# Kernel optimization log

Measured on AMD Instinct MI355X. Metric: run time of the kernel, lower is better.

Reference implementation:

```python
import jax, jax.numpy as jnp
import numpy as np

N = 100000      # nodes
E = 1600000     # edges (avg degree 16)
IN_DIM = 256
HID = 128
EPS = 0.3


def setup_inputs() -> dict:
    key = jax.random.key(0)
    ks = jax.random.split(key, 6)
    x = jax.random.normal(ks[0], (N, IN_DIM), dtype=jnp.float32)
    # edges without self-loops (dst = src + nonzero offset mod N)
    src = jax.random.randint(ks[1], (E,), 0, N)
    off = jax.random.randint(ks[2], (E,), 1, N)
    dst = (src + off) % N
    edge_index = jnp.stack([src, dst]).astype(jnp.int32)
    # xavier_normal_ with gain=1.414 for t1 and gate
    g1 = 1.414 * np.sqrt(2.0 / (IN_DIM + HID))
    w1 = (jax.random.normal(ks[3], (HID, IN_DIM)) * g1).astype(jnp.float32)
    b1 = jnp.zeros((HID,), jnp.float32)
    gg = 1.414 * np.sqrt(2.0 / (2 * HID + 1))
    gate_w = (jax.random.normal(ks[4], (1, 2 * HID)) * gg).astype(jnp.float32)
    gate_b = jnp.zeros((1,), jnp.float32)
    return dict(x=x, edge_index=edge_index, w1=w1, b1=b1, gate_w=gate_w, gate_b=gate_b)


def reference(x, edge_index, w1, b1, gate_w, gate_b):
    src, dst = edge_index[0], edge_index[1]
    # in-degree based symmetric norm, deg clamped to >= 1
    deg = jax.ops.segment_sum(jnp.ones((E,), jnp.float32), dst, num_segments=N)
    norm = jnp.clip(deg, 1.0) ** -0.5  # [N]

    h = jax.nn.relu(x @ w1.T + b1)     # [N, HID] (dropout p=0 / eval -> identity)
    raw = h

    # gate([h_dst, h_src]) decomposed: concat @ W^T = h_dst @ w_d + h_src @ w_s
    w_d, w_s = gate_w[0, :HID], gate_w[0, HID:]
    a_dst = h @ w_d                    # [N]
    a_src = h @ w_s                    # [N]
    g = jnp.tanh(a_dst[dst] + a_src[src] + gate_b[0])   # [E] per-edge gate
    e = g * norm[dst] * norm[src]                        # [E]

    # u_mul_e + sum: gather src features, weight, scatter-add to dst
    z = jax.ops.segment_sum(h[src] * e[:, None], dst, num_segments=N)  # [N, HID]
    return EPS * raw + z
```

## Files before the change

### kernel.cpp

```cpp
#include <hip/hip_runtime.h>
#include <math.h>
#include <stdint.h>

#define N_NODES 100000
#define N_EDGES 1600000
#define IN_DIM  256
#define HID     128
#define EPS_C   0.3f

#define NPB      128
#define NBKT     782
#define NBKT_P   784
#define BCAP     3072
#define S1_CHUNK 4096
#define S1_BLOCKS 391
#define GC(b)    ((b) * 16)

#define PK_SRC(p)  ((p) & 0x1FFFF)
#define PK_LI(p)   ((p) >> 17)

typedef __attribute__((ext_vector_type(8))) __bf16 bf16x8;
typedef __attribute__((ext_vector_type(4))) float  f32x4;
typedef __attribute__((ext_vector_type(8))) unsigned short ushort8;

static __device__ __forceinline__ unsigned short f2bf(float f) {
    unsigned u = __float_as_uint(f);
    unsigned r = (u + 0x7fffu + ((u >> 16) & 1u)) >> 16;
    return (unsigned short)r;
}
static __device__ __forceinline__ float bf2f(unsigned short s) {
    return __uint_as_float((unsigned)s << 16);
}
static __device__ __forceinline__ float fast_tanh(float x) {
    float e = __builtin_exp2f(x * 2.8853900817779268f);
    return 1.0f - 2.0f / (e + 1.0f);
}

__global__ __launch_bounds__(256) void convert_w1_kernel(const float* __restrict__ w1,
                                                         unsigned short* __restrict__ w1b) {
    int i = blockIdx.x * 256 + threadIdx.x;
    if (i * 4 >= HID * IN_DIM) return;
    float4 v = *(const float4*)&w1[i * 4];
    ushort4 r;
    r.x = f2bf(v.x); r.y = f2bf(v.y); r.z = f2bf(v.z); r.w = f2bf(v.w);
    *(ushort4*)&w1b[i * 4] = r;
}

__global__ __launch_bounds__(512) void partition_kernel(const int* __restrict__ src,
                                                        const int* __restrict__ dst,
                                                        int* __restrict__ gcur,
                                                        int* __restrict__ ebuf) {
    __shared__ int hist[NBKT_P];
    __shared__ int cur[NBKT_P];

    int t = threadIdx.x;
    for (int i = t; i < NBKT_P; i += 512) hist[i] = 0;
    __syncthreads();

    int base4 = blockIdx.x * (S1_CHUNK / 4);
    int rem4  = N_EDGES / 4 - base4;

    int4 sv[2], dv[2];
#pragma unroll
    for (int j = 0; j < 2; j++) {
        int i4 = j * 512 + t;
        if (i4 < rem4) {
            sv[j] = *(const int4*)&src[(base4 + i4) * 4];
            dv[j] = *(const int4*)&dst[(base4 + i4) * 4];
        } else {
            dv[j] = make_int4(-1, -1, -1, -1);
        }
    }
#pragma unroll
    for (int j = 0; j < 2; j++) {
        if (dv[j].x >= 0) {
            atomicAdd(&hist[dv[j].x >> 7], 1);
            atomicAdd(&hist[dv[j].y >> 7], 1);
            atomicAdd(&hist[dv[j].z >> 7], 1);
            atomicAdd(&hist[dv[j].w >> 7], 1);
        }
    }
    __syncthreads();

    if (t < NBKT_P / 2) {
        int h0 = hist[2 * t], h1 = hist[2 * t + 1];
        if (h0 > 0) cur[2 * t]     = atomicAdd(&gcur[GC(2 * t)], h0);
        if (h1 > 0) cur[2 * t + 1] = atomicAdd(&gcur[GC(2 * t + 1)], h1);
    }
    __syncthreads();

#pragma unroll
    for (int j = 0; j < 2; j++) {
        if (dv[j].x >= 0) {
            int b, p;
            b = dv[j].x >> 7; p = atomicAdd(&cur[b], 1);
            if (p < BCAP) ebuf[(size_t)b * BCAP + p] = ((dv[j].x & (NPB - 1)) << 17) | sv[j].x;
            b = dv[j].y >> 7; p = atomicAdd(&cur[b], 1);
            if (p < BCAP) ebuf[(size_t)b * BCAP + p] = ((dv[j].y & (NPB - 1)) << 17) | sv[j].y;
            b = dv[j].z >> 7; p = atomicAdd(&cur[b], 1);
            if (p < BCAP) ebuf[(size_t)b * BCAP + p] = ((dv[j].z & (NPB - 1)) << 17) | sv[j].z;
            b = dv[j].w >> 7; p = atomicAdd(&cur[b], 1);
            if (p < BCAP) ebuf[(size_t)b * BCAP + p] = ((dv[j].w & (NPB - 1)) << 17) | sv[j].w;
        }
    }
}

__global__ __launch_bounds__(512) void deg_kernel(const int* __restrict__ gcur,
                                                  const int* __restrict__ ebuf,
                                                  int2* __restrict__ rs2,
                                                  float* __restrict__ nrm) {
    __shared__ int dcnt[NPB];
    __shared__ int s[NPB];
    int b = blockIdx.x;
    int t = threadIdx.x;
    if (t < NPB) dcnt[t] = 0;
    __syncthreads();

    int ecnt = gcur[GC(b)];
    if (ecnt > BCAP) ecnt = BCAP;
    for (int j = t; j < ecnt; j += 512)
        atomicAdd(&dcnt[PK_LI(ebuf[(size_t)b * BCAP + j])], 1);
    __syncthreads();

    int v = 0;
    if (t < NPB) { v = dcnt[t]; s[t] = v; }
    __syncthreads();
    for (int off = 1; off < NPB; off <<= 1) {
        int a = (t < NPB && t >= off) ? s[t - off] : 0;
        __syncthreads();
        if (t < NPB) s[t] += a;
        __syncthreads();
    }

    int nbase = b * NPB;
    int nn = N_NODES - nbase;
    if (nn > NPB) nn = NPB;
    if (t < nn) {
        int incl = s[t];
        rs2[nbase + t] = make_int2(b * BCAP + incl - v, b * BCAP + incl);
        nrm[nbase + t] = rsqrtf(fmaxf((float)v, 1.0f));
    }
}

__global__ __launch_bounds__(512, 4) void gemm_kernel(const float* __restrict__ x,
                                                      const unsigned short* __restrict__ w1b,
                                                      const float* __restrict__ b1,
                                                      const float* __restrict__ gw,
                                                      const float* __restrict__ nrm,
                                                      unsigned short* __restrict__ h,
                                                      float2* __restrict__ pd_pack,
                                                      float2* __restrict__ ps_pack) {
    __shared__ unsigned short Bs[HID * IN_DIM];

    int tid  = threadIdx.x;
    int bm   = blockIdx.x * 128;
    int wv   = tid >> 6;
    int lane = tid & 63;
    int col  = lane & 15;
    int kq   = lane >> 4;

    {
        int n  = tid >> 2;
        int c0 = tid & 3;
        const unsigned short* srcp = &w1b[n * IN_DIM];
#pragma unroll
        for (int j = 0; j < 8; j++) {
            int c = c0 + 4 * j;
            *(ushort8*)((char*)Bs + n * 512 + ((c ^ (n & 7)) * 16)) =
                *(const ushort8*)&srcp[c * 8];
        }
    }

    f32x4 acc[8];
#pragma unroll
    for (int nf = 0; nf < 8; nf++) acc[nf] = (f32x4){0.f, 0.f, 0.f, 0.f};

    int row  = bm + wv * 16 + col;
    bool rok = row < N_NODES;
    const float* ap = &x[(size_t)row * IN_DIM + kq * 8];

    bf16x8 af[8];
#pragma unroll
    for (int i = 0; i < 8; i++) {
        float4 a0 = {0, 0, 0, 0}, a1 = {0, 0, 0, 0};
        if (rok) {
            a0 = *(const float4*)(ap + 32 * i);
            a1 = *(const float4*)(ap + 32 * i + 4);
        }
        ushort8 av;
        av[0] = f2bf(a0.x); av[1] = f2bf(a0.y); av[2] = f2bf(a0.z); av[3] = f2bf(a0.w);
        av[4] = f2bf(a1.x); av[5] = f2bf(a1.y); av[6] = f2bf(a1.z); av[7] = f2bf(a1.w);
        af[i] = *(bf16x8*)&av;
    }

    __syncthreads();

#pragma unroll
    for (int i = 0; i < 8; i++) {
        int swz = (4 * i + kq) ^ (col & 7);
#pragma unroll
        for (int nf = 0; nf < 8; nf++) {
            int n = nf * 16 + col;
            bf16x8 bfrag = *(bf16x8*)((char*)Bs + n * 512 + swz * 16);
            acc[nf] = __builtin_amdgcn_mfma_f32_16x16x32_bf16(af[i], bfrag, acc[nf], 0, 0, 0);
        }
    }

    float bias[8], wd[8], wsv[8];
#pragma unroll
    for (int nf = 0; nf < 8; nf++) {
        bias[nf] = b1[nf * 16 + col];
        wd[nf]   = gw[nf * 16 + col];
        wsv[nf]  = gw[HID + nf * 16 + col];
    }
#pragma unroll
    for (int r = 0; r < 4; r++) {
        int gm = bm + wv * 16 + kq * 4 + r;
        float pd = 0.f, ps = 0.f;
        bool ok = (gm < N_NODES);
#pragma unroll
        for (int nf = 0; nf < 8; nf++) {
            float v = fmaxf(acc[nf][r] + bias[nf], 0.f);
            pd = fmaf(v, wd[nf], pd);
            ps = fmaf(v, wsv[nf], ps);
            if (ok) h[(size_t)gm * HID + nf * 16 + col] = f2bf(v);
        }
#pragma unroll
        for (int m = 1; m < 16; m <<= 1) {
            pd += __shfl_xor(pd, m);
            ps += __shfl_xor(ps, m);
        }
        if (ok && col == 0) {
            float nv = nrm[gm];
            pd_pack[gm] = make_float2(pd, nv);
            ps_pack[gm] = make_float2(ps, nv);
        }
    }
}

__global__ __launch_bounds__(512) void scatter2_kernel(const int* __restrict__ gcur,
                                                       const int* __restrict__ ebuf,
                                                       const int2* __restrict__ rs2,
                                                       const float2* __restrict__ pd_pack,
                                                       const float2* __restrict__ ps_pack,
                                                       const float* __restrict__ gb,
                                                       int2* __restrict__ epack) {
    __shared__ int    curs[NPB];
    __shared__ float2 pdl[NPB];
    int b = blockIdx.x;
    int t = threadIdx.x;
    int nbase = b * NPB;
    int nn = N_NODES - nbase;
    if (nn > NPB) nn = NPB;
    if (t < nn) {
        curs[t] = rs2[nbase + t].x;
        pdl[t]  = pd_pack[nbase + t];
    }
    __syncthreads();

    int ecnt = gcur[GC(b)];
    if (ecnt > BCAP) ecnt = BCAP;
    float gbv = gb[0];
    for (int j = t; j < ecnt; j += 512) {
        int p = ebuf[(size_t)b * BCAP + j];
        int s  = PK_SRC(p);
        int li = PK_LI(p);
        int pos = atomicAdd(&curs[li], 1);
        float2 pdp = pdl[li];
        float2 psp = ps_pack[s];
        float g = fast_tanh(pdp.x + psp.x + gbv);
        epack[pos] = make_int2(s, __float_as_int(g * pdp.y * psp.y));
    }
}

__global__ __launch_bounds__(256) void aggregate_kernel(const int2* __restrict__ rs2,
                                                        const int2* __restrict__ epack,
                                                        const unsigned short* __restrict__ h,
                                                        float* __restrict__ out) {
    int node = blockIdx.x * 4 + (threadIdx.x >> 6);
    if (node >= N_NODES) return;
    int lane = threadIdx.x & 63;
    int q  = lane >> 4;
    int ql = lane & 15;

    int2 be = rs2[node];
    int beg = be.x;
    int end = be.y;

    float acc[8];
#pragma unroll
    for (int t = 0; t < 8; t++) acc[t] = 0.f;

    int j = beg;
    for (; j + 8 <= end; j += 8) {
        int2 e0 = epack[j + q];
        int2 e1 = epack[j + 4 + q];
        ushort8 r0 = *(const ushort8*)&h[(size_t)e0.x * HID + ql * 8];
        ushort8 r1 = *(const ushort8*)&h[(size_t)e1.x * HID + ql * 8];
        float c0 = __int_as_float(e0.y);
        float c1 = __int_as_float(e1.y);
#pragma unroll
        for (int t = 0; t < 8; t++) {
            acc[t] = fmaf(c0, bf2f(r0[t]), acc[t]);
            acc[t] = fmaf(c1, bf2f(r1[t]), acc[t]);
        }
    }
    for (; j < end; j += 4) {
        bool act = (j + q) < end;
        int idx = act ? (j + q) : beg;
        int2 e = epack[idx];
        ushort8 r = *(const ushort8*)&h[(size_t)e.x * HID + ql * 8];
        float c = act ? __int_as_float(e.y) : 0.f;
#pragma unroll
        for (int t = 0; t < 8; t++) acc[t] = fmaf(c, bf2f(r[t]), acc[t]);
    }
#pragma unroll
    for (int t = 0; t < 8; t++) {
        acc[t] += __shfl_xor(acc[t], 16);
        acc[t] += __shfl_xor(acc[t], 32);
    }
    if (q == 0) {
        ushort8 hd = *(const ushort8*)&h[(size_t)node * HID + ql * 8];
        f32x4 o0, o1;
        o0.x = fmaf(EPS_C, bf2f(hd[0]), acc[0]);
        o0.y = fmaf(EPS_C, bf2f(hd[1]), acc[1]);
        o0.z = fmaf(EPS_C, bf2f(hd[2]), acc[2]);
        o0.w = fmaf(EPS_C, bf2f(hd[3]), acc[3]);
        o1.x = fmaf(EPS_C, bf2f(hd[4]), acc[4]);
        o1.y = fmaf(EPS_C, bf2f(hd[5]), acc[5]);
        o1.z = fmaf(EPS_C, bf2f(hd[6]), acc[6]);
        o1.w = fmaf(EPS_C, bf2f(hd[7]), acc[7]);
        __builtin_nontemporal_store(o0, (f32x4*)&out[(size_t)node * HID + ql * 8]);
        __builtin_nontemporal_store(o1, (f32x4*)&out[(size_t)node * HID + ql * 8 + 4]);
    }
}

extern "C" void kernel_launch(void* const* d_in, const int* in_sizes, int n_in,
                              void* d_out, int out_size, void* d_ws, size_t ws_size,
                              hipStream_t stream) {
    const float* x  = (const float*)d_in[0];
    const int*   ei = (const int*)d_in[1];
    const float* w1 = (const float*)d_in[2];
    const float* b1 = (const float*)d_in[3];
    const float* gw = (const float*)d_in[4];
    const float* gb = (const float*)d_in[5];
    float* out = (float*)d_out;

    const int* src = ei;
    const int* dst = ei + N_EDGES;

    uintptr_t base = (uintptr_t)d_ws;
    size_t off = 0;
    auto alloc = [&](size_t bytes) -> void* {
        void* p = (void*)(base + off);
        off += (bytes + 255) & ~(size_t)255;
        return p;
    };
    unsigned short* h   = (unsigned short*)alloc((size_t)N_NODES * HID * 2);
    float2* pd_pack     = (float2*)alloc((size_t)N_NODES * 8);
    float2* ps_pack     = (float2*)alloc((size_t)N_NODES * 8);
    float*  nrm         = (float*)alloc((size_t)N_NODES * 4);
    int2*   rs2         = (int2*)alloc((size_t)N_NODES * 8);
    int2*   epack       = (int2*)alloc((size_t)NBKT * BCAP * 8);
    unsigned short* w1b = (unsigned short*)alloc((size_t)HID * IN_DIM * 2);
    int*    gcur        = (int*)alloc((size_t)NBKT * 16 * 4);
    int*    ebuf        = (int*)alloc((size_t)NBKT * BCAP * 4);

    (void)hipMemsetAsync(gcur, 0, (size_t)NBKT * 16 * 4, stream);

    convert_w1_kernel<<<(HID * IN_DIM / 4 + 255) / 256, 256, 0, stream>>>(w1, w1b);
    partition_kernel<<<S1_BLOCKS, 512, 0, stream>>>(src, dst, gcur, ebuf);
    deg_kernel<<<NBKT, 512, 0, stream>>>(gcur, ebuf, rs2, nrm);
    gemm_kernel<<<(N_NODES + 127) / 128, 512, 0, stream>>>(x, w1b, b1, gw, nrm,
                                                           h, pd_pack, ps_pack);
    scatter2_kernel<<<NBKT, 512, 0, stream>>>(gcur, ebuf, rs2,
                                              pd_pack, ps_pack, gb, epack);
    aggregate_kernel<<<(N_NODES + 3) / 4, 256, 0, stream>>>(rs2, epack, h, out);
}
```

Before: 304.7 us.

## Fuse edge scatter with aggregation in LDS and drop GEMM weight staging

Merges the per-bucket edge-weight scatter and neighbour aggregation into one kernel. Each 1024-thread block sorts its bucket's edges into shared memory and then aggregates its 128 nodes directly, so the global epack buffer and one launch go away. Separately, the GEMM no longer stages W1 in LDS; it reads B fragments straight from global/L2 with 64-row blocks of 256 threads. The trade-offs are lower occupancy from large blocks with a 24KB LDS buffer, and repeated uncoalesced global weight reads in the GEMM.

```diff
diff --git a/kernel.cpp b/kernel.cpp
--- a/kernel.cpp
+++ b/kernel.cpp
@@ -142,38 +142,20 @@
     }
 }
 
-__global__ __launch_bounds__(512, 4) void gemm_kernel(const float* __restrict__ x,
-                                                      const unsigned short* __restrict__ w1b,
-                                                      const float* __restrict__ b1,
-                                                      const float* __restrict__ gw,
-                                                      const float* __restrict__ nrm,
-                                                      unsigned short* __restrict__ h,
-                                                      float2* __restrict__ pd_pack,
-                                                      float2* __restrict__ ps_pack) {
-    __shared__ unsigned short Bs[HID * IN_DIM];
-
+__global__ __launch_bounds__(256) void gemm_kernel(const float* __restrict__ x,
+                                                   const unsigned short* __restrict__ w1b,
+                                                   const float* __restrict__ b1,
+                                                   const float* __restrict__ gw,
+                                                   const float* __restrict__ nrm,
+                                                   unsigned short* __restrict__ h,
+                                                   float2* __restrict__ pd_pack,
+                                                   float2* __restrict__ ps_pack) {
     int tid  = threadIdx.x;
-    int bm   = blockIdx.x * 128;
+    int bm   = blockIdx.x * 64;
     int wv   = tid >> 6;
     int lane = tid & 63;
     int col  = lane & 15;
     int kq   = lane >> 4;
-
-    {
-        int n  = tid >> 2;
-        int c0 = tid & 3;
-        const unsigned short* srcp = &w1b[n * IN_DIM];
-#pragma unroll
-        for (int j = 0; j < 8; j++) {
-            int c = c0 + 4 * j;
-            *(ushort8*)((char*)Bs + n * 512 + ((c ^ (n & 7)) * 16)) =
-                *(const ushort8*)&srcp[c * 8];
-        }
-    }
-
-    f32x4 acc[8];
-#pragma unroll
-    for (int nf = 0; nf < 8; nf++) acc[nf] = (f32x4){0.f, 0.f, 0.f, 0.f};
 
     int row  = bm + wv * 16 + col;
     bool rok = row < N_NODES;
@@ -193,15 +175,15 @@
         af[i] = *(bf16x8*)&av;
     }
 
-    __syncthreads();
+    f32x4 acc[8];
+#pragma unroll
+    for (int nf = 0; nf < 8; nf++) acc[nf] = (f32x4){0.f, 0.f, 0.f, 0.f};
 
 #pragma unroll
     for (int i = 0; i < 8; i++) {
-        int swz = (4 * i + kq) ^ (col & 7);
 #pragma unroll
         for (int nf = 0; nf < 8; nf++) {
-            int n = nf * 16 + col;
-            bf16x8 bfrag = *(bf16x8*)((char*)Bs + n * 512 + swz * 16);
+            bf16x8 bfrag = *(const bf16x8*)&w1b[(nf * 16 + col) * IN_DIM + i * 32 + kq * 8];
             acc[nf] = __builtin_amdgcn_mfma_f32_16x16x32_bf16(af[i], bfrag, acc[nf], 0, 0, 0);
         }
     }
@@ -238,100 +220,114 @@
     }
 }
 
-__global__ __launch_bounds__(512) void scatter2_kernel(const int* __restrict__ gcur,
-                                                       const int* __restrict__ ebuf,
-                                                       const int2* __restrict__ rs2,
-                                                       const float2* __restrict__ pd_pack,
-                                                       const float2* __restrict__ ps_pack,
-                                                       const float* __restrict__ gb,
-                                                       int2* __restrict__ epack) {
+__global__ __launch_bounds__(1024) void spagg2_kernel(const int* __restrict__ gcur,
+                                                      const int* __restrict__ ebuf,
+                                                      const int2* __restrict__ rs2,
+                                                      const float2* __restrict__ pd_pack,
+                                                      const float2* __restrict__ ps_pack,
+                                                      const float* __restrict__ gb,
+                                                      const unsigned short* __restrict__ h,
+                                                      float* __restrict__ out) {
+    __shared__ int2   sorted[BCAP];
     __shared__ int    curs[NPB];
+    __shared__ int    begs[NPB];
+    __shared__ int    ends[NPB];
     __shared__ float2 pdl[NPB];
+
     int b = blockIdx.x;
     int t = threadIdx.x;
     int nbase = b * NPB;
-    int nn = N_NODES - nbase;
-    if (nn > NPB) nn = NPB;
-    if (t < nn) {
-        curs[t] = rs2[nbase + t].x;
-        pdl[t]  = pd_pack[nbase + t];
+
+    if (t < NPB) {
+        int node = nbase + t;
+        if (node < N_NODES) {
+            int2 r = rs2[node];
+            int lb = r.x - b * BCAP;
+            begs[t] = lb; curs[t] = lb;
+            ends[t] = r.y - b * BCAP;
+            pdl[t]  = pd_pack[node];
+        } else {
+            begs[t] = 0; curs[t] = 0; ends[t] = 0;
+            pdl[t] = make_float2(0.f, 0.f);
+        }
     }
     __syncthreads();
 
     int ecnt = gcur[GC(b)];
     if (ecnt > BCAP) ecnt = BCAP;
     float gbv = gb[0];
-    for (int j = t; j < ecnt; j += 512) {
-        int p = ebuf[(size_t)b * BCAP + j];
+
+    for (int j = t; j < ecnt; j += 1024) {
+        int p  = ebuf[(size_t)b * BCAP + j];
         int s  = PK_SRC(p);
         int li = PK_LI(p);
         int pos = atomicAdd(&curs[li], 1);
         float2 pdp = pdl[li];
         float2 psp = ps_pack[s];
-        float g = fast_tanh(pdp.x + psp.x + gbv);
-        epack[pos] = make_int2(s, __float_as_int(g * pdp.y * psp.y));
-    }
-}
-
-__global__ __launch_bounds__(256) void aggregate_kernel(const int2* __restrict__ rs2,
-                                                        const int2* __restrict__ epack,
-                                                        const unsigned short* __restrict__ h,
-                                                        float* __restrict__ out) {
-    int node = blockIdx.x * 4 + (threadIdx.x >> 6);
-    if (node >= N_NODES) return;
-    int lane = threadIdx.x & 63;
+        float g = fast_tanh(pdp.x + psp.x + gbv) * pdp.y * psp.y;
+        sorted[pos] = make_int2(s, __float_as_int(g));
+    }
+    __syncthreads();
+
+    int lane = t & 63;
+    int w    = t >> 6;
     int q  = lane >> 4;
     int ql = lane & 15;
 
-    int2 be = rs2[node];
-    int beg = be.x;
-    int end = be.y;
-
-    float acc[8];
-#pragma unroll
-    for (int t = 0; t < 8; t++) acc[t] = 0.f;
-
-    int j = beg;
-    for (; j + 8 <= end; j += 8) {
-        int2 e0 = epack[j + q];
-        int2 e1 = epack[j + 4 + q];
-        ushort8 r0 = *(const ushort8*)&h[(size_t)e0.x * HID + ql * 8];
-        ushort8 r1 = *(const ushort8*)&h[(size_t)e1.x * HID + ql * 8];
-        float c0 = __int_as_float(e0.y);
-        float c1 = __int_as_float(e1.y);
-#pragma unroll
-        for (int t = 0; t < 8; t++) {
-            acc[t] = fmaf(c0, bf2f(r0[t]), acc[t]);
-            acc[t] = fmaf(c1, bf2f(r1[t]), acc[t]);
-        }
-    }
-    for (; j < end; j += 4) {
-        bool act = (j + q) < end;
-        int idx = act ? (j + q) : beg;
-        int2 e = epack[idx];
-        ushort8 r = *(const ushort8*)&h[(size_t)e.x * HID + ql * 8];
-        float c = act ? __int_as_float(e.y) : 0.f;
-#pragma unroll
-        for (int t = 0; t < 8; t++) acc[t] = fmaf(c, bf2f(r[t]), acc[t]);
-    }
-#pragma unroll
-    for (int t = 0; t < 8; t++) {
-        acc[t] += __shfl_xor(acc[t], 16);
-        acc[t] += __shfl_xor(acc[t], 32);
-    }
-    if (q == 0) {
-        ushort8 hd = *(const ushort8*)&h[(size_t)node * HID + ql * 8];
-        f32x4 o0, o1;
-        o0.x = fmaf(EPS_C, bf2f(hd[0]), acc[0]);
-        o0.y = fmaf(EPS_C, bf2f(hd[1]), acc[1]);
-        o0.z = fmaf(EPS_C, bf2f(hd[2]), acc[2]);
-        o0.w = fmaf(EPS_C, bf2f(hd[3]), acc[3]);
-        o1.x = fmaf(EPS_C, bf2f(hd[4]), acc[4]);
-        o1.y = fmaf(EPS_C, bf2f(hd[5]), acc[5]);
-        o1.z = fmaf(EPS_C, bf2f(hd[6]), acc[6]);
-        o1.w = fmaf(EPS_C, bf2f(hd[7]), acc[7]);
-        __builtin_nontemporal_store(o0, (f32x4*)&out[(size_t)node * HID + ql * 8]);
-        __builtin_nontemporal_store(o1, (f32x4*)&out[(size_t)node * HID + ql * 8 + 4]);
+#pragma unroll
+    for (int k = 0; k < NPB / 16; k++) {
+        int li = w + 16 * k;
+        int node = nbase + li;
+        if (node >= N_NODES) continue;
+        int beg = begs[li];
+        int end = ends[li];
+
+        float acc[8];
+#pragma unroll
+        for (int u = 0; u < 8; u++) acc[u] = 0.f;
+
+        int j = beg;
+        for (; j + 8 <= end; j += 8) {
+            int2 e0 = sorted[j + q];
+            int2 e1 = sorted[j + 4 + q];
+            ushort8 r0 = *(const ushort8*)&h[(size_t)e0.x * HID + ql * 8];
+            ushort8 r1 = *(const ushort8*)&h[(size_t)e1.x * HID + ql * 8];
+            float c0 = __int_as_float(e0.y);
+            float c1 = __int_as_float(e1.y);
+#pragma unroll
+            for (int u = 0; u < 8; u++) {
+                acc[u] = fmaf(c0, bf2f(r0[u]), acc[u]);
+                acc[u] = fmaf(c1, bf2f(r1[u]), acc[u]);
+            }
+        }
+        for (; j < end; j += 4) {
+            bool act = (j + q) < end;
+            int idx = act ? (j + q) : beg;
+            int2 e = sorted[idx];
+            ushort8 r = *(const ushort8*)&h[(size_t)e.x * HID + ql * 8];
+            float c = act ? __int_as_float(e.y) : 0.f;
+#pragma unroll
+            for (int u = 0; u < 8; u++) acc[u] = fmaf(c, bf2f(r[u]), acc[u]);
+        }
+#pragma unroll
+        for (int u = 0; u < 8; u++) {
+            acc[u] += __shfl_xor(acc[u], 16);
+            acc[u] += __shfl_xor(acc[u], 32);
+        }
+        if (q == 0) {
+            ushort8 hd = *(const ushort8*)&h[(size_t)node * HID + ql * 8];
+            f32x4 o0, o1;
+            o0.x = fmaf(EPS_C, bf2f(hd[0]), acc[0]);
+            o0.y = fmaf(EPS_C, bf2f(hd[1]), acc[1]);
+            o0.z = fmaf(EPS_C, bf2f(hd[2]), acc[2]);
+            o0.w = fmaf(EPS_C, bf2f(hd[3]), acc[3]);
+            o1.x = fmaf(EPS_C, bf2f(hd[4]), acc[4]);
+            o1.y = fmaf(EPS_C, bf2f(hd[5]), acc[5]);
+            o1.z = fmaf(EPS_C, bf2f(hd[6]), acc[6]);
+            o1.w = fmaf(EPS_C, bf2f(hd[7]), acc[7]);
+            __builtin_nontemporal_store(o0, (f32x4*)&out[(size_t)node * HID + ql * 8]);
+            __builtin_nontemporal_store(o1, (f32x4*)&out[(size_t)node * HID + ql * 8 + 4]);
+        }
     }
 }
 
@@ -361,7 +357,6 @@
     float2* ps_pack     = (float2*)alloc((size_t)N_NODES * 8);
     float*  nrm         = (float*)alloc((size_t)N_NODES * 4);
     int2*   rs2         = (int2*)alloc((size_t)N_NODES * 8);
-    int2*   epack       = (int2*)alloc((size_t)NBKT * BCAP * 8);
     unsigned short* w1b = (unsigned short*)alloc((size_t)HID * IN_DIM * 2);
     int*    gcur        = (int*)alloc((size_t)NBKT * 16 * 4);
     int*    ebuf        = (int*)alloc((size_t)NBKT * BCAP * 4);
@@ -371,9 +366,8 @@
     convert_w1_kernel<<<(HID * IN_DIM / 4 + 255) / 256, 256, 0, stream>>>(w1, w1b);
     partition_kernel<<<S1_BLOCKS, 512, 0, stream>>>(src, dst, gcur, ebuf);
     deg_kernel<<<NBKT, 512, 0, stream>>>(gcur, ebuf, rs2, nrm);
-    gemm_kernel<<<(N_NODES + 127) / 128, 512, 0, stream>>>(x, w1b, b1, gw, nrm,
-                                                           h, pd_pack, ps_pack);
-    scatter2_kernel<<<NBKT, 512, 0, stream>>>(gcur, ebuf, rs2,
-                                              pd_pack, ps_pack, gb, epack);
-    aggregate_kernel<<<(N_NODES + 3) / 4, 256, 0, stream>>>(rs2, epack, h, out);
-}
+    gemm_kernel<<<(N_NODES + 63) / 64, 256, 0, stream>>>(x, w1b, b1, gw, nrm,
+                                                         h, pd_pack, ps_pack);
+    spagg2_kernel<<<NBKT, 1024, 0, stream>>>(gcur, ebuf, rs2,
+                                             pd_pack, ps_pack, gb, h, out);
+}
```

New measurement: 337.6 us. 1.11x slower.
